# Kernel tuning notes

Hardware: AMD Instinct MI355X
Metric: run time of the kernel (lower is better)

## Reference

```python
import jax, jax.numpy as jnp
import numpy as np

B, S, D = 4, 1024, 768
V, L, K = 50265, 256, 4
COMMIT = 0.25
PERP_W = 0.1


def _l2n(a):
    return a * jax.lax.rsqrt(jnp.sum(a * a, axis=-1, keepdims=True) + 1e-12)


def setup_inputs() -> dict:
    key = jax.random.key(0)
    ks = jax.random.split(key, 4)
    return {
        'x': jax.random.normal(ks[0], (B, S, D), dtype=jnp.float32),
        'codebook': jax.random.normal(ks[1], (V, D), dtype=jnp.float32) * 0.02,
        'W_in': jax.random.normal(ks[2], (D, L), dtype=jnp.float32) / np.sqrt(D),
        'b_in': jnp.zeros((L,), dtype=jnp.float32),
        'W_code': jax.random.normal(ks[3], (D, L), dtype=jnp.float32) / np.sqrt(D),
        'b_code': jnp.zeros((L,), dtype=jnp.float32),
    }


def reference(x, codebook, W_in, b_in, W_code, b_code):
    # project inputs and codebook to latent space, L2-normalize
    zi = _l2n(x.reshape(-1, D) @ W_in + b_in)                 # [N, L]
    # original normalizes latent codebook twice (idempotent) then stop-grads
    zc = jax.lax.stop_gradient(_l2n(codebook @ W_code + b_code))  # [V, L]
    # squared euclidean distance: |a|^2 + |b|^2 - 2 a.b
    d = (jnp.sum(zi * zi, -1, keepdims=True)
         + jnp.sum(zc * zc, -1)[None, :]
         - 2.0 * (zi @ zc.T)).reshape(B, S, V)                # [B, S, V]
    # top-k nearest codes (exact top_k as reference for approx_min_k)
    idx = jax.lax.top_k(-d, K)[1]                             # [B, S, K] int32
    # quantize: gather codes and average over k (top_k_avg path)
    quantized = jnp.take(codebook, idx, axis=0).mean(axis=-2) # [B, S, D]
    # codebook stats without materializing [B,S,K,V] one-hot
    counts = jnp.zeros((V,), x.dtype).at[idx.reshape(-1)].add(1.0)
    codebook_usage = jnp.sum(counts > 0).astype(x.dtype) / V / K
    avg_probs = counts / (B * S * K)
    log_perp = -jnp.sum(avg_probs * jnp.log(avg_probs + 1e-10))
    perplexity = jnp.exp(log_perp)
    # train losses (quantized is stop-gradient'd before loss in original)
    q_sg = jax.lax.stop_gradient(quantized)

    def train_loss(q, t):
        e = jnp.mean((jax.lax.stop_gradient(q) - t) ** 2) * COMMIT
        ql = jnp.mean((q - jax.lax.stop_gradient(t)) ** 2)
        return e + ql

    loss = train_loss(q_sg, x)
    loss = loss + train_loss(q_sg @ W_code + b_code, x @ W_in + b_in)
    loss = loss + PERP_W * log_perp
    # straight-through estimator
    out = x + jax.lax.stop_gradient(q_sg - x)
    return out, loss, perplexity, codebook_usage
```

## Files before the change

### kernel.cpp

```cpp
#include <hip/hip_runtime.h>
#include <math.h>

#define N_TOK 4096
#define DDIM  768
#define LDIM  256
#define VNUM  50265
#define VPAD  50304
#define NT64  786
#define NGRP  16
#define QBLK  256
#define KSEL  4
#define M3    3145728

#define WS_ZI_PRE 0
#define WS_ZI     (WS_ZI_PRE + N_TOK*LDIM)
#define WS_ZIB    (WS_ZI + N_TOK*LDIM)
#define WS_ZC     (WS_ZIB + N_TOK*LDIM/2)
#define WS_ZCB    (WS_ZC + VPAD*LDIM)
#define WS_QUANT  WS_ZCB
#define WS_CAND   (WS_ZCB + VPAD*LDIM/2)
#define WS_IDX    (WS_CAND + N_TOK*64)
#define WS_COUNTS (WS_IDX + N_TOK*4)
#define WS_ACCUM  (WS_COUNTS + VPAD)

typedef __attribute__((ext_vector_type(8))) short short8;
typedef __attribute__((ext_vector_type(4))) float f32x4;

__device__ __forceinline__ unsigned short f2bf(float f) {
    unsigned u = __float_as_uint(f);
    u += 0x7fffu + ((u >> 16) & 1u);
    return (unsigned short)(u >> 16);
}

__device__ __forceinline__ bool better(float v1, int i1, float v2, int i2) {
    return (v1 > v2) || (v1 == v2 && i1 < i2);
}

template<int K>
__device__ __forceinline__ void insertK(float (&v)[K], int (&ix)[K], float nv, int ni) {
    if (!better(nv, ni, v[K-1], ix[K-1])) return;
    v[K-1] = nv; ix[K-1] = ni;
    #pragma unroll
    for (int j = K-1; j > 0; j--) {
        if (better(v[j], ix[j], v[j-1], ix[j-1])) {
            float tv = v[j]; v[j] = v[j-1]; v[j-1] = tv;
            int ti = ix[j]; ix[j] = ix[j-1]; ix[j-1] = ti;
        } else break;
    }
}

__global__ __launch_bounds__(256) void gemm_k(
    const float* __restrict__ A, const float* __restrict__ W,
    const float* __restrict__ bias, float* __restrict__ out_pre,
    float* __restrict__ out_norm, unsigned short* __restrict__ out_bf,
    const float* __restrict__ target, float* __restrict__ accum_slot,
    int M, int mode)
{
    __shared__ float a_s[32*64];
    __shared__ float w_s[32*256];
    const int tid = threadIdx.x;
    const int tx = tid & 31, ty = tid >> 5;
    const int mbase = blockIdx.x * 64;

    float acc[8][8];
    #pragma unroll
    for (int i = 0; i < 8; i++)
        #pragma unroll
        for (int j = 0; j < 8; j++) acc[i][j] = 0.f;

    for (int kk = 0; kk < DDIM; kk += 32) {
        __syncthreads();
        #pragma unroll
        for (int s = 0; s < 2; s++) {
            int slot = tid + s*256;
            int row = slot >> 3, kc = (slot & 7) << 2;
            int gr = mbase + row; if (gr >= M) gr = M - 1;
            float4 v = *(const float4*)&A[(size_t)gr*DDIM + kk + kc];
            a_s[(kc+0)*64 + row] = v.x;
            a_s[(kc+1)*64 + row] = v.y;
            a_s[(kc+2)*64 + row] = v.z;
            a_s[(kc+3)*64 + row] = v.w;
        }
        #pragma unroll
        for (int s = 0; s < 8; s++) {
            int slot = tid + s*256;
            int r = slot >> 6, c = (slot & 63) << 2;
            *(float4*)&w_s[r*256 + c] = *(const float4*)&W[(size_t)(kk + r)*LDIM + c];
        }
        __syncthreads();
        #pragma unroll
        for (int k = 0; k < 32; k++) {
            float4 a0 = *(float4*)&a_s[k*64 + ty*8];
            float4 a1 = *(float4*)&a_s[k*64 + ty*8 + 4];
            float4 w0 = *(float4*)&w_s[k*256 + tx*4];
            float4 w1 = *(float4*)&w_s[k*256 + 128 + tx*4];
            float am[8] = {a0.x,a0.y,a0.z,a0.w,a1.x,a1.y,a1.z,a1.w};
            float wn[8] = {w0.x,w0.y,w0.z,w0.w,w1.x,w1.y,w1.z,w1.w};
            #pragma unroll
            for (int i = 0; i < 8; i++)
                #pragma unroll
                for (int j = 0; j < 8; j++)
                    acc[i][j] = fmaf(am[i], wn[j], acc[i][j]);
        }
    }

    float bn[8];
    #pragma unroll
    for (int j = 0; j < 8; j++) {
        int col = (j < 4) ? (tx*4 + j) : (128 + tx*4 + (j-4));
        bn[j] = bias[col];
    }
    #pragma unroll
    for (int i = 0; i < 8; i++)
        #pragma unroll
        for (int j = 0; j < 8; j++) acc[i][j] += bn[j];

    if (mode == 1) {
        #pragma unroll
        for (int i = 0; i < 8; i++) {
            int gr = mbase + ty*8 + i;
            if (gr < M) {
                *(float4*)&out_pre[(size_t)gr*LDIM + tx*4] =
                    make_float4(acc[i][0], acc[i][1], acc[i][2], acc[i][3]);
                *(float4*)&out_pre[(size_t)gr*LDIM + 128 + tx*4] =
                    make_float4(acc[i][4], acc[i][5], acc[i][6], acc[i][7]);
            }
        }
    }
    if (mode == 1 || mode == 2) {
        #pragma unroll
        for (int i = 0; i < 8; i++) {
            float s = 0.f;
            #pragma unroll
            for (int j = 0; j < 8; j++) s += acc[i][j]*acc[i][j];
            #pragma unroll
            for (int m = 16; m >= 1; m >>= 1) s += __shfl_xor(s, m, 64);
            float sc = 1.0f / sqrtf(s + 1e-12f);
            int gr = mbase + ty*8 + i;
            bool wr = (mode == 2) || (gr < M);
            if (wr) {
                float p[8];
                #pragma unroll
                for (int j = 0; j < 8; j++) p[j] = acc[i][j]*sc;
                *(float4*)&out_norm[(size_t)gr*LDIM + tx*4] = make_float4(p[0],p[1],p[2],p[3]);
                *(float4*)&out_norm[(size_t)gr*LDIM + 128 + tx*4] = make_float4(p[4],p[5],p[6],p[7]);
                if (out_bf) {
                    ushort4 b0, b1;
                    b0.x = f2bf(p[0]); b0.y = f2bf(p[1]); b0.z = f2bf(p[2]); b0.w = f2bf(p[3]);
                    b1.x = f2bf(p[4]); b1.y = f2bf(p[5]); b1.z = f2bf(p[6]); b1.w = f2bf(p[7]);
                    if (mode == 1) {
                        *(ushort4*)&out_bf[(size_t)gr*LDIM + tx*4] = b0;
                        *(ushort4*)&out_bf[(size_t)gr*LDIM + 128 + tx*4] = b1;
                    } else {
                        const int T = gr >> 6, c = gr & 63;
                        #pragma unroll
                        for (int h = 0; h < 2; h++) {
                            const int k0 = h*128 + tx*4;
                            const int kc = k0 >> 6, seg = (k0 >> 3) & 7, e = k0 & 7;
                            const int slot = c*8 + (seg ^ (c & 7));
                            size_t idx = ((size_t)(T*4 + kc))*4096 + slot*8 + e;
                            *(ushort4*)&out_bf[idx] = h ? b1 : b0;
                        }
                    }
                }
            }
        }
    }
    if (mode == 3) {
        float ls = 0.f;
        #pragma unroll
        for (int i = 0; i < 8; i++) {
            int gr = mbase + ty*8 + i;
            if (gr < M) {
                #pragma unroll
                for (int j = 0; j < 8; j++) {
                    int col = (j < 4) ? (tx*4 + j) : (128 + tx*4 + (j-4));
                    float dd = acc[i][j] - target[(size_t)gr*LDIM + col];
                    ls = fmaf(dd, dd, ls);
                }
            }
        }
        #pragma unroll
        for (int off = 32; off >= 1; off >>= 1) ls += __shfl_down(ls, off, 64);
        __syncthreads();
        if ((tid & 63) == 0) a_s[tid >> 6] = ls;
        __syncthreads();
        if (tid == 0) atomicAdd(accum_slot, a_s[0]+a_s[1]+a_s[2]+a_s[3]);
    }
}

__global__ __launch_bounds__(512, 2) __attribute__((amdgpu_waves_per_eu(2, 2)))
void filter_kernel(
    const unsigned short* __restrict__ zib, const unsigned short* __restrict__ zcb,
    int* __restrict__ cand)
{
    __shared__ unsigned short lds[2*4096];
    const int tid = threadIdx.x;
    const int wave = tid >> 6, lane = tid & 63;
    const int l15 = lane & 15, l4 = lane >> 4;
    const int qbase = blockIdx.x * QBLK + wave * 32;
    const int g = blockIdx.y;

    short8 afrag[2][8];
    #pragma unroll
    for (int qt = 0; qt < 2; qt++)
        #pragma unroll
        for (int ks = 0; ks < 8; ks++)
            afrag[qt][ks] = *(const short8*)&zib[(size_t)(qbase + qt*16 + l15)*LDIM + ks*32 + l4*8];

    float tv[2][4][3]; int tix[2][4][3];
    #pragma unroll
    for (int qt = 0; qt < 2; qt++)
        #pragma unroll
        for (int rr = 0; rr < 4; rr++)
            #pragma unroll
            for (int j = 0; j < 3; j++) { tv[qt][rr][j] = -1e30f; tix[qt][rr][j] = 0x7fffffff; }

    f32x4 acc[2][4];
    #pragma unroll
    for (int qt = 0; qt < 2; qt++)
        #pragma unroll
        for (int tc = 0; tc < 4; tc++) acc[qt][tc] = (f32x4)(0.f);

    const int nct = (g < 2) ? 50 : 49;
    const int NCk = nct * 4;

    #define CHUNK_OFF(ci) ((size_t)((g + ((ci) >> 2)*NGRP)*4 + ((ci) & 3)) * 4096)

    uint4 breg = *(const uint4*)&zcb[CHUNK_OFF(0) + tid*8];
    *(uint4*)&lds[tid*8] = breg;
    breg = *(const uint4*)&zcb[CHUNK_OFF(1) + tid*8];
    __syncthreads();

    for (int ci = 0; ci < NCk; ci++) {
        const unsigned short* lb = &lds[(ci & 1)*4096];
        #pragma unroll
        for (int ks2 = 0; ks2 < 2; ks2++) {
            const int kf = (ci & 3)*2 + ks2;
            #pragma unroll
            for (int tc = 0; tc < 4; tc++) {
                const int c = tc*16 + l15;
                const int slot = c*8 + ((ks2*4 + l4) ^ (c & 7));
                const short8 b = *(const short8*)&lb[slot*8];
                acc[0][tc] = __builtin_amdgcn_mfma_f32_16x16x32_bf16(afrag[0][kf], b, acc[0][tc], 0, 0, 0);
                acc[1][tc] = __builtin_amdgcn_mfma_f32_16x16x32_bf16(afrag[1][kf], b, acc[1][tc], 0, 0, 0);
            }
        }

        if ((ci & 3) == 3) {
            const int T = g + (ci >> 2)*NGRP;
            #pragma unroll
            for (int tc = 0; tc < 4; tc++) {
                const int col = T*64 + tc*16 + l15;
                const bool ok = col < VNUM;
                #pragma unroll
                for (int qt = 0; qt < 2; qt++) {
                    #pragma unroll
                    for (int rr = 0; rr < 4; rr++) {
                        float v = acc[qt][tc][rr];
                        if (ok) insertK<3>(tv[qt][rr], tix[qt][rr], v, col);
                    }
                    acc[qt][tc] = (f32x4)(0.f);
                }
            }
        }

        __syncthreads();
        if (ci + 1 < NCk) {
            *(uint4*)&lds[((ci+1) & 1)*4096 + tid*8] = breg;
            if (ci + 2 < NCk) breg = *(const uint4*)&zcb[CHUNK_OFF(ci+2) + tid*8];
            __syncthreads();
        }
    }
    #undef CHUNK_OFF

    #pragma unroll
    for (int qt = 0; qt < 2; qt++)
        #pragma unroll
        for (int rr = 0; rr < 4; rr++) {
            float mv[4] = { tv[qt][rr][0], tv[qt][rr][1], tv[qt][rr][2], -1e30f };
            int   mi[4] = { tix[qt][rr][0], tix[qt][rr][1], tix[qt][rr][2], 0x7fffffff };
            #pragma unroll
            for (int m = 1; m < 16; m <<= 1) {
                float ov[4]; int oi[4];
                #pragma unroll
                for (int s = 0; s < 4; s++) {
                    ov[s] = __shfl_xor(mv[s], m, 64);
                    oi[s] = __shfl_xor(mi[s], m, 64);
                }
                #pragma unroll
                for (int s = 0; s < 4; s++) insertK<4>(mv, mi, ov[s], oi[s]);
            }
            if (l15 == 0) {
                const int q = qbase + qt*16 + l4*4 + rr;
                #pragma unroll
                for (int j = 0; j < 4; j++) cand[(size_t)q*64 + g*4 + j] = mi[j];
            }
        }
}

__global__ __launch_bounds__(256) void rescore_kernel(
    const float* __restrict__ zi, const float* __restrict__ zc,
    const int* __restrict__ cand, int* __restrict__ idx4)
{
    __shared__ float zi_s[256];
    __shared__ float sval[64];
    __shared__ int   sidx[64];
    const int q = blockIdx.x;
    const int t = threadIdx.x;
    if (t < 64) *(float4*)&zi_s[t*4] = *(const float4*)&zi[(size_t)q*LDIM + t*4];
    __syncthreads();

    const int j = t >> 2, l4 = t & 3;
    int idx = cand[(size_t)q*64 + j];
    const bool valid = (unsigned)idx < (unsigned)VNUM;
    const float* r = zc + (size_t)(valid ? idx : 0)*LDIM;
    float dot = 0.f, nsq = 0.f;
    #pragma unroll
    for (int i = 0; i < 16; i++) {
        float4 v = *(const float4*)&r[i*16 + l4*4];
        float4 z = *(const float4*)&zi_s[i*16 + l4*4];
        dot = fmaf(v.x, z.x, fmaf(v.y, z.y, fmaf(v.z, z.z, fmaf(v.w, z.w, dot))));
        nsq = fmaf(v.x, v.x, fmaf(v.y, v.y, fmaf(v.z, v.z, fmaf(v.w, v.w, nsq))));
    }
    dot += __shfl_xor(dot, 1, 64); dot += __shfl_xor(dot, 2, 64);
    nsq += __shfl_xor(nsq, 1, 64); nsq += __shfl_xor(nsq, 2, 64);
    const float sc = valid ? (dot - 0.5f*nsq) : -1e30f;
    if (l4 == 0) { sval[j] = sc; sidx[j] = valid ? idx : 0x7fffffff; }
    __syncthreads();

    if (t < 64) {
        float v[4] = {-1e30f, -1e30f, -1e30f, -1e30f};
        int ix[4] = {0x7fffffff, 0x7fffffff, 0x7fffffff, 0x7fffffff};
        insertK<4>(v, ix, sval[t], sidx[t]);
        #pragma unroll
        for (int m = 1; m < 64; m <<= 1) {
            float ov[4]; int oi[4];
            #pragma unroll
            for (int s = 0; s < 4; s++) {
                ov[s] = __shfl_xor(v[s], m, 64);
                oi[s] = __shfl_xor(ix[s], m, 64);
            }
            #pragma unroll
            for (int s = 0; s < 4; s++) insertK<4>(v, ix, ov[s], oi[s]);
        }
        if (t == 0) {
            #pragma unroll
            for (int s = 0; s < 4; s++) idx4[q*4 + s] = ix[s];
        }
    }
}

__global__ __launch_bounds__(192) void gather_kernel(
    const float* __restrict__ x, const float* __restrict__ cb,
    const int* __restrict__ idx4, float* __restrict__ quant,
    float* __restrict__ out, float* __restrict__ counts,
    float* __restrict__ accum)
{
    __shared__ float red[3];
    const int n = blockIdx.x;
    const int t = threadIdx.x;
    const int i0 = idx4[n*4+0], i1 = idx4[n*4+1], i2 = idx4[n*4+2], i3 = idx4[n*4+3];
    if (t < 4) atomicAdd(&counts[idx4[n*4+t]], 1.0f);
    const int d = t*4;
    float4 c0 = *(const float4*)&cb[(size_t)i0*DDIM + d];
    float4 c1 = *(const float4*)&cb[(size_t)i1*DDIM + d];
    float4 c2 = *(const float4*)&cb[(size_t)i2*DDIM + d];
    float4 c3 = *(const float4*)&cb[(size_t)i3*DDIM + d];
    float4 xv = *(const float4*)&x[(size_t)n*DDIM + d];
    float4 qv;
    qv.x = (((c0.x + c1.x) + c2.x) + c3.x) * 0.25f;
    qv.y = (((c0.y + c1.y) + c2.y) + c3.y) * 0.25f;
    qv.z = (((c0.z + c1.z) + c2.z) + c3.z) * 0.25f;
    qv.w = (((c0.w + c1.w) + c2.w) + c3.w) * 0.25f;
    float4 o;
    o.x = xv.x + (qv.x - xv.x);
    o.y = xv.y + (qv.y - xv.y);
    o.z = xv.z + (qv.z - xv.z);
    o.w = xv.w + (qv.w - xv.w);
    *(float4*)&quant[(size_t)n*DDIM + d] = qv;
    *(float4*)&out[(size_t)n*DDIM + d] = o;
    float d0 = qv.x - xv.x, d1 = qv.y - xv.y, d2 = qv.z - xv.z, d3 = qv.w - xv.w;
    float ls = d0*d0 + d1*d1 + d2*d2 + d3*d3;
    #pragma unroll
    for (int off = 32; off >= 1; off >>= 1) ls += __shfl_down(ls, off, 64);
    if ((t & 63) == 0) red[t >> 6] = ls;
    __syncthreads();
    if (t == 0) atomicAdd(accum, red[0] + red[1] + red[2]);
}

__global__ __launch_bounds__(256) void stats_kernel(
    const float* __restrict__ counts, float* __restrict__ accum)
{
    __shared__ float redE[4], redN[4];
    int v = blockIdx.x*256 + threadIdx.x;
    float ent = 0.f, nnz = 0.f;
    if (v < VNUM) {
        float c = counts[v];
        if (c > 0.f) {
            float p = c * (1.0f/16384.0f);
            ent = p * logf(p + 1e-10f);
            nnz = 1.f;
        }
    }
    #pragma unroll
    for (int off = 32; off >= 1; off >>= 1) {
        ent += __shfl_down(ent, off, 64);
        nnz += __shfl_down(nnz, off, 64);
    }
    int t = threadIdx.x;
    if ((t & 63) == 0) { redE[t>>6] = ent; redN[t>>6] = nnz; }
    __syncthreads();
    if (t == 0) {
        atomicAdd(accum+2, redE[0]+redE[1]+redE[2]+redE[3]);
        atomicAdd(accum+3, redN[0]+redN[1]+redN[2]+redN[3]);
    }
}

__global__ void final_kernel(const float* __restrict__ accum, float* __restrict__ out)
{
    float logp = -accum[2];
    float m1 = accum[0] * (1.0f / (float)M3);
    float m2 = accum[1] * (1.0f / (float)(N_TOK*LDIM));
    float loss = (m1*0.25f + m1) + (m2*0.25f + m2) + 0.1f*logp;
    out[M3+0] = loss;
    out[M3+1] = expf(logp);
    out[M3+2] = (accum[3] / (float)VNUM) / (float)KSEL;
}

extern "C" void kernel_launch(void* const* d_in, const int* in_sizes, int n_in,
                              void* d_out, int out_size, void* d_ws, size_t ws_size,
                              hipStream_t stream)
{
    const float* x      = (const float*)d_in[0];
    const float* cb     = (const float*)d_in[1];
    const float* W_in   = (const float*)d_in[2];
    const float* b_in   = (const float*)d_in[3];
    const float* W_code = (const float*)d_in[4];
    const float* b_code = (const float*)d_in[5];
    float* out = (float*)d_out;
    float* w   = (float*)d_ws;

    float* zi_pre = w + WS_ZI_PRE;
    float* zi     = w + WS_ZI;
    unsigned short* zib = (unsigned short*)(w + WS_ZIB);
    float* zc     = w + WS_ZC;
    unsigned short* zcb = (unsigned short*)(w + WS_ZCB);
    float* quant  = w + WS_QUANT;
    int*   cand   = (int*)(w + WS_CAND);
    int*   idx4   = (int*)(w + WS_IDX);
    float* counts = w + WS_COUNTS;
    float* accum  = w + WS_ACCUM;

    hipMemsetAsync(counts, 0, (VPAD + 8)*sizeof(float), stream);

    gemm_k<<<N_TOK/64, 256, 0, stream>>>(x, W_in, b_in, zi_pre, zi, zib,
                                         nullptr, nullptr, N_TOK, 1);
    gemm_k<<<VPAD/64, 256, 0, stream>>>(cb, W_code, b_code, nullptr, zc, zcb,
                                        nullptr, nullptr, VNUM, 2);
    filter_kernel<<<dim3(N_TOK/QBLK, NGRP), 512, 0, stream>>>(zib, zcb, cand);
    rescore_kernel<<<N_TOK, 256, 0, stream>>>(zi, zc, cand, idx4);
    gather_kernel<<<N_TOK, 192, 0, stream>>>(x, cb, idx4, quant, out, counts, accum);
    stats_kernel<<<(VNUM + 255)/256, 256, 0, stream>>>(counts, accum);
    gemm_k<<<N_TOK/64, 256, 0, stream>>>(quant, W_code, b_code, nullptr, nullptr, nullptr,
                                         zi_pre, accum+1, N_TOK, 3);
    final_kernel<<<1, 1, 0, stream>>>(accum, out);
}
```

Before: 1.240 ms.

## Halve filter block size and make the top-3 insertion branchless

The filter kernel now runs 256-thread blocks, each covering 128 queries instead of 256. This doubles the grid to 512 blocks so more work is spread across CUs, and each thread stages two uint4 codebook chunks per LDS tile instead of one. The per-lane top-3 insertion is replaced by a select-based ins3 that avoids divergent compare-and-swap loops. Out-of-range columns are handled by feeding a sentinel value instead of branching. The cost is that every block still streams its whole codebook group, so total codebook reads from L2 and memory double.

Measured after the change: 1.056 ms. 1.17x faster.

```diff
diff --git a/kernel.cpp b/kernel.cpp
--- a/kernel.cpp
+++ b/kernel.cpp
@@ -8,7 +8,7 @@
 #define VPAD  50304
 #define NT64  786
 #define NGRP  16
-#define QBLK  256
+#define QBLK  128
 #define KSEL  4
 #define M3    3145728
 
@@ -47,6 +47,16 @@
             int ti = ix[j]; ix[j] = ix[j-1]; ix[j-1] = ti;
         } else break;
     }
+}
+
+__device__ __forceinline__ void ins3(float (&v)[3], int (&ix)[3], float nv, int ni) {
+    bool c2 = nv > v[2], c1 = nv > v[1], c0 = nv > v[0];
+    v[2]  = c1 ? v[1]  : (c2 ? nv : v[2]);
+    ix[2] = c1 ? ix[1] : (c2 ? ni : ix[2]);
+    v[1]  = c0 ? v[0]  : (c1 ? nv : v[1]);
+    ix[1] = c0 ? ix[0] : (c1 ? ni : ix[1]);
+    v[0]  = c0 ? nv : v[0];
+    ix[0] = c0 ? ni : ix[0];
 }
 
 __global__ __launch_bounds__(256) void gemm_k(
@@ -189,8 +199,7 @@
     }
 }
 
-__global__ __launch_bounds__(512, 2) __attribute__((amdgpu_waves_per_eu(2, 2)))
-void filter_kernel(
+__global__ __launch_bounds__(256, 2) void filter_kernel(
     const unsigned short* __restrict__ zib, const unsigned short* __restrict__ zcb,
     int* __restrict__ cand)
 {
@@ -227,9 +236,13 @@
 
     #define CHUNK_OFF(ci) ((size_t)((g + ((ci) >> 2)*NGRP)*4 + ((ci) & 3)) * 4096)
 
-    uint4 breg = *(const uint4*)&zcb[CHUNK_OFF(0) + tid*8];
-    *(uint4*)&lds[tid*8] = breg;
-    breg = *(const uint4*)&zcb[CHUNK_OFF(1) + tid*8];
+    uint4 br0, br1;
+    br0 = *(const uint4*)&zcb[CHUNK_OFF(0) + tid*8];
+    br1 = *(const uint4*)&zcb[CHUNK_OFF(0) + 2048 + tid*8];
+    *(uint4*)&lds[tid*8] = br0;
+    *(uint4*)&lds[2048 + tid*8] = br1;
+    br0 = *(const uint4*)&zcb[CHUNK_OFF(1) + tid*8];
+    br1 = *(const uint4*)&zcb[CHUNK_OFF(1) + 2048 + tid*8];
     __syncthreads();
 
     for (int ci = 0; ci < NCk; ci++) {
@@ -257,8 +270,8 @@
                 for (int qt = 0; qt < 2; qt++) {
                     #pragma unroll
                     for (int rr = 0; rr < 4; rr++) {
-                        float v = acc[qt][tc][rr];
-                        if (ok) insertK<3>(tv[qt][rr], tix[qt][rr], v, col);
+                        float v = ok ? acc[qt][tc][rr] : -1e30f;
+                        ins3(tv[qt][rr], tix[qt][rr], v, col);
                     }
                     acc[qt][tc] = (f32x4)(0.f);
                 }
@@ -267,8 +280,12 @@
 
         __syncthreads();
         if (ci + 1 < NCk) {
-            *(uint4*)&lds[((ci+1) & 1)*4096 + tid*8] = breg;
-            if (ci + 2 < NCk) breg = *(const uint4*)&zcb[CHUNK_OFF(ci+2) + tid*8];
+            *(uint4*)&lds[((ci+1) & 1)*4096 + tid*8] = br0;
+            *(uint4*)&lds[((ci+1) & 1)*4096 + 2048 + tid*8] = br1;
+            if (ci + 2 < NCk) {
+                br0 = *(const uint4*)&zcb[CHUNK_OFF(ci+2) + tid*8];
+                br1 = *(const uint4*)&zcb[CHUNK_OFF(ci+2) + 2048 + tid*8];
+            }
             __syncthreads();
         }
     }
@@ -458,7 +475,7 @@
                                          nullptr, nullptr, N_TOK, 1);
     gemm_k<<<VPAD/64, 256, 0, stream>>>(cb, W_code, b_code, nullptr, zc, zcb,
                                         nullptr, nullptr, VNUM, 2);
-    filter_kernel<<<dim3(N_TOK/QBLK, NGRP), 512, 0, stream>>>(zib, zcb, cand);
+    filter_kernel<<<dim3(N_TOK/QBLK, NGRP), 256, 0, stream>>>(zib, zcb, cand);
     rescore_kernel<<<N_TOK, 256, 0, stream>>>(zi, zc, cand, idx4);
     gather_kernel<<<N_TOK, 192, 0, stream>>>(x, cb, idx4, quant, out, counts, accum);
     stats_kernel<<<(VNUM + 255)/256, 256, 0, stream>>>(counts, accum);
```
